# Optimization experiments

Measured on AMD Instinct MI355X. Metric: run time of the kernel, lower is better.

## Reference

```python
import jax, jax.numpy as jnp
import numpy as np

HEADS = 16  # module init arg `heads`


def setup_inputs() -> dict:
    key = jax.random.key(0)
    k1, k2, k3 = jax.random.split(key, 3)
    B, T, D = 2, 2048, 1024
    x = jax.random.normal(k1, (B, T, D), dtype=jnp.float32)
    w_qkv = jax.random.normal(k2, (D, 3 * D), dtype=jnp.float32) * (1.0 / np.sqrt(D))
    w_proj = jax.random.normal(k3, (D, D), dtype=jnp.float32) * (1.0 / np.sqrt(D))
    b_proj = jnp.zeros((D,), dtype=jnp.float32)
    return {"x": x, "w_qkv": w_qkv, "w_proj": w_proj, "b_proj": b_proj,
            "window": 16, "stride": 16}


def reference(x, w_qkv, w_proj, b_proj, window, stride):
    B, T, D = x.shape
    H = HEADS
    hd = D // H
    scale = 1.0 / np.sqrt(hd)

    qkv = x @ w_qkv                              # [B,T,3D]
    qkv = qkv.reshape(B, T, 3, H, hd)
    q = jnp.transpose(qkv[:, :, 0], (0, 2, 1, 3))  # [B,H,T,hd]
    k = jnp.transpose(qkv[:, :, 1], (0, 2, 1, 3))
    v = jnp.transpose(qkv[:, :, 2], (0, 2, 1, 3))

    # Local window attention: pad front with zeros (matches F.pad), gather
    # sliding windows so patches[..., t, w, :] = k_padded[..., t + w, :].
    pad = window - 1
    k_pad = jnp.pad(k, ((0, 0), (0, 0), (pad, 0), (0, 0)))
    v_pad = jnp.pad(v, ((0, 0), (0, 0), (pad, 0), (0, 0)))
    win_idx = jnp.arange(T)[:, None] + jnp.arange(window)[None, :]  # [T,W]
    pk = k_pad[:, :, win_idx]                    # [B,H,T,W,hd]
    pv = v_pad[:, :, win_idx]                    # [B,H,T,W,hd]

    attn_local = jnp.einsum('bhtd,bhtwd->bhtw', q, pk) * scale
    attn_local = jax.nn.softmax(attn_local, axis=-1)  # zero-pad keys included, as in torch
    out_local = jnp.einsum('bhtw,bhtwd->bhtd', attn_local, pv)

    # Strided global attention
    g_idx = jnp.arange(0, T, stride)
    kg = k[:, :, g_idx]                          # [B,H,G,hd]
    vg = v[:, :, g_idx]
    attn_g = jnp.einsum('bhtd,bhgd->bhtg', q, kg) * scale
    attn_g = jax.nn.softmax(attn_g, axis=-1)
    out_global = jnp.einsum('bhtg,bhgd->bhtd', attn_g, vg)

    out = out_local + out_global                 # [B,H,T,hd]
    out = jnp.transpose(out, (0, 2, 1, 3)).reshape(B, T, D)
    return out @ w_proj + b_proj
```

## Files before the change

### kernel.cpp

```cpp
#include <hip/hip_runtime.h>
#include <hip/hip_bf16.h>

#define BB 2
#define TT 2048
#define DD 1024
#define HH 16
#define HD 64
#define WIN 16
#define NG 128
#define QKVLD 3072

typedef __bf16 bf16x8 __attribute__((ext_vector_type(8)));
typedef float f32x4 __attribute__((ext_vector_type(4)));
typedef _Float16 h2 __attribute__((ext_vector_type(2)));

__device__ __forceinline__ unsigned short f2bf(float f) {
    union { float f; unsigned int i; } x; x.f = f;
    unsigned int r = x.i + 0x7FFFu + ((x.i >> 16) & 1u);
    return (unsigned short)(r >> 16);
}
__device__ __forceinline__ unsigned short f2h(float f) {
    union { _Float16 h; unsigned short u; } x; x.h = (_Float16)f; return x.u;
}
__device__ __forceinline__ h2 shfl_h2(h2 v, int mask) {
    union { h2 h; int i; } X; X.h = v;
    X.i = __shfl_xor(X.i, mask, 64);
    return X.h;
}

#if defined(__has_builtin)
#  if __has_builtin(__builtin_amdgcn_fdot2)
#    define DOT2(a, b, c) __builtin_amdgcn_fdot2((a), (b), (c), false)
#  endif
#endif
#ifndef DOT2
#  define DOT2(a, b, c) ((c) + (float)(a).x * (float)(b).x + (float)(a).y * (float)(b).y)
#endif

__device__ __forceinline__ void gll16(const unsigned short* g, unsigned short* l) {
    __builtin_amdgcn_global_load_lds(
        (const __attribute__((address_space(1))) void*)g,
        (__attribute__((address_space(3))) void*)l,
        16, 0, 0);
}

__global__ __launch_bounds__(256) void prepass_kernel(
    const float* __restrict__ x,
    const float* __restrict__ w_qkv,
    const float* __restrict__ w_proj,
    unsigned short* __restrict__ xb,
    unsigned short* __restrict__ wqkvT,
    unsigned short* __restrict__ wprojT)
{
    __shared__ float tile[64][65];
    const int bid = blockIdx.x;
    const int tid = threadIdx.x;

    if (bid < 2048) {
        const size_t i = ((size_t)bid * 256 + tid) * 8;
        float4 f0 = *(const float4*)(x + i);
        float4 f1 = *(const float4*)(x + i + 4);
        ushort4 a = { f2bf(f0.x), f2bf(f0.y), f2bf(f0.z), f2bf(f0.w) };
        ushort4 b = { f2bf(f1.x), f2bf(f1.y), f2bf(f1.z), f2bf(f1.w) };
        *(ushort4*)(xb + i) = a;
        *(ushort4*)(xb + i + 4) = b;
        return;
    }

    const float* w;
    unsigned short* wT;
    int nblk, kblk, N;
    if (bid < 2816) {
        const int b2 = bid - 2048;
        w = w_qkv; wT = wqkvT; N = 3072;
        nblk = b2 % 48; kblk = b2 / 48;
    } else {
        const int b2 = bid - 2816;
        w = w_proj; wT = wprojT; N = 1024;
        nblk = b2 % 16; kblk = b2 / 16;
    }
    const int K = 1024;
    const int n0 = nblk * 64, k0 = kblk * 64;

    {
        const int krow = tid >> 2;
        const int nc0  = (tid & 3) * 16;
        const float* src = w + (size_t)(k0 + krow) * N + n0 + nc0;
        float4 f0 = *(const float4*)(src);
        float4 f1 = *(const float4*)(src + 4);
        float4 f2 = *(const float4*)(src + 8);
        float4 f3 = *(const float4*)(src + 12);
        *(float4*)&tile[krow][nc0]      = f0;
        *(float4*)&tile[krow][nc0 + 4]  = f1;
        *(float4*)&tile[krow][nc0 + 8]  = f2;
        *(float4*)&tile[krow][nc0 + 12] = f3;
    }
    __syncthreads();
    #pragma unroll
    for (int rep = 0; rep < 2; ++rep) {
        const int n   = (tid >> 3) + rep * 32;
        const int kc0 = (tid & 7) * 8;
        union { uint4 v; unsigned short u[8]; } o;
        #pragma unroll
        for (int j = 0; j < 8; ++j) o.u[j] = f2bf(tile[kc0 + j][n]);
        *(uint4*)(wT + (size_t)(n0 + n) * K + k0 + kc0) = o.v;
    }
}

template<int MODE, int TN>
__global__ __launch_bounds__(256) void gemm_kernel(
    const unsigned short* __restrict__ A,
    const unsigned short* __restrict__ Bt,
    void* __restrict__ Cp,
    const float* __restrict__ bias,
    int M, int N, int K)
{
    constexpr int NJ = TN / 32;
    constexpr int BR = TN / 4;
    __shared__ __align__(16) unsigned short As[128 * 32];
    __shared__ __align__(16) unsigned short Bs[TN * 32];
    const int tid  = threadIdx.x;
    const int wave = tid >> 6;
    const int lane = tid & 63;
    const int lm   = lane & 15;
    const int quad = lane >> 4;
    const int wm   = (wave >> 1) * 64;
    const int wn   = (wave & 1) * (TN / 2);
    const int bm   = blockIdx.y * 128;
    const int bn   = blockIdx.x * TN;

    f32x4 acc[4][NJ];
    const f32x4 z4 = { 0.f, 0.f, 0.f, 0.f };
    #pragma unroll
    for (int i = 0; i < 4; ++i)
        #pragma unroll
        for (int j = 0; j < NJ; ++j) acc[i][j] = z4;

    const int lrow = lane >> 2, lcol = (lane & 3) * 8;
    const unsigned short* gA0 = A  + (size_t)(bm + wave * 32 + lrow) * K + lcol;
    const unsigned short* gA1 = gA0 + (size_t)16 * K;
    const unsigned short* gB0 = Bt + (size_t)(bn + wave * BR + lrow) * K + lcol;
    const unsigned short* gB1 = gB0 + (size_t)16 * K;
    unsigned short* lA0 = &As[(wave * 32) * 32];
    unsigned short* lA1 = &As[(wave * 32 + 16) * 32];
    unsigned short* lB0 = &Bs[(wave * BR) * 32];
    unsigned short* lB1 = &Bs[(wave * BR + 16) * 32];

    for (int k0 = 0; k0 < K; k0 += 32) {
        __syncthreads();
        gll16(gA0 + k0, lA0);
        gll16(gA1 + k0, lA1);
        gll16(gB0 + k0, lB0);
        if constexpr (BR == 32) gll16(gB1 + k0, lB1);
        __syncthreads();
        bf16x8 af[4], bfr[NJ];
        #pragma unroll
        for (int i = 0; i < 4; ++i)
            af[i] = *(const bf16x8*)&As[(wm + i * 16 + lm) * 32 + quad * 8];
        #pragma unroll
        for (int j = 0; j < NJ; ++j)
            bfr[j] = *(const bf16x8*)&Bs[(wn + j * 16 + lm) * 32 + quad * 8];
        #pragma unroll
        for (int i = 0; i < 4; ++i)
            #pragma unroll
            for (int j = 0; j < NJ; ++j)
                acc[i][j] = __builtin_amdgcn_mfma_f32_16x16x32_bf16(
                    af[i], bfr[j], acc[i][j], 0, 0, 0);
    }

    #pragma unroll
    for (int i = 0; i < 4; ++i) {
        #pragma unroll
        for (int r = 0; r < 4; ++r) {
            const int row = bm + wm + i * 16 + quad * 4 + r;
            #pragma unroll
            for (int j = 0; j < NJ; ++j) {
                const int col = bn + wn + j * 16 + lm;
                float v = acc[i][j][r];
                if constexpr (MODE == 0) {
                    ((unsigned short*)Cp)[(size_t)row * N + col] = f2h(v);
                } else {
                    ((float*)Cp)[(size_t)row * N + col] = v + bias[col];
                }
            }
        }
    }
}

__global__ __launch_bounds__(256) void attn_kernel(
    const unsigned short* __restrict__ qkv,
    unsigned short* __restrict__ attn_out)
{
    __shared__ __align__(16) unsigned short smem[72 * (2 * 128 + 2 * 47)];
    unsigned short* Kg = smem;
    unsigned short* Vg = smem + 128 * 72;
    unsigned short* Kl = smem + 2 * 128 * 72;
    unsigned short* Vl = Kl + 47 * 72;

    const int tid   = threadIdx.x;
    const int bx    = blockIdx.x;
    const int chunk = bx & 63;
    const int bh    = bx >> 6;
    const int b     = bh >> 4;
    const int h     = bh & 15;
    const int t0    = chunk * 32;
    const int qloc  = tid >> 3;
    const int ks    = tid & 7;
    const int tq    = t0 + qloc;

    const size_t rowK = (size_t)(b * TT) * QKVLD + 1024 + h * HD;

    {
        const int r = tid >> 1, hfi = tid & 1;
        const int g = ((r & 15) << 3) | (r >> 4);
        const unsigned short* kr = qkv + rowK + (size_t)g * 16 * QKVLD + hfi * 32;
        const unsigned short* vr = kr + 1024;
        unsigned short* kd = Kg + r * 72 + hfi * 32;
        unsigned short* vd = Vg + r * 72 + hfi * 32;
        #pragma unroll
        for (int j = 0; j < 4; ++j) {
            *(uint4*)(kd + j * 8) = *(const uint4*)(kr + j * 8);
            *(uint4*)(vd + j * 8) = *(const uint4*)(vr + j * 8);
        }
        if (r < 47) {
            const int t = t0 + r - 15;
            unsigned short* kld = Kl + r * 72 + hfi * 32;
            unsigned short* vld = Vl + r * 72 + hfi * 32;
            if (t < 0) {
                uint4 z = { 0, 0, 0, 0 };
                #pragma unroll
                for (int j = 0; j < 4; ++j) { *(uint4*)(kld + j * 8) = z; *(uint4*)(vld + j * 8) = z; }
            } else {
                const unsigned short* klr = qkv + rowK + (size_t)t * QKVLD + hfi * 32;
                const unsigned short* vlr = klr + 1024;
                #pragma unroll
                for (int j = 0; j < 4; ++j) {
                    *(uint4*)(kld + j * 8) = *(const uint4*)(klr + j * 8);
                    *(uint4*)(vld + j * 8) = *(const uint4*)(vlr + j * 8);
                }
            }
        }
    }

    h2 qh[32];
    {
        const unsigned short* qrow = qkv + (size_t)(b * TT + tq) * QKVLD + h * HD;
        const h2 sc = { (_Float16)0.125f, (_Float16)0.125f };
        #pragma unroll
        for (int i = 0; i < 8; ++i) {
            union { uint4 u; h2 hh[4]; } U;
            U.u = *(const uint4*)(qrow + i * 8);
            qh[4 * i + 0] = U.hh[0] * sc; qh[4 * i + 1] = U.hh[1] * sc;
            qh[4 * i + 2] = U.hh[2] * sc; qh[4 * i + 3] = U.hh[3] * sc;
        }
    }

    __syncthreads();

    auto score = [&](const unsigned short* kp) -> float {
        float s0 = 0.f, s1 = 0.f, s2 = 0.f, s3 = 0.f;
        #pragma unroll
        for (int c = 0; c < 8; ++c) {
            union { uint4 u; h2 hh[4]; } U;
            U.u = *(const uint4*)(kp + c * 8);
            s0 = DOT2(U.hh[0], qh[4 * c + 0], s0);
            s1 = DOT2(U.hh[1], qh[4 * c + 1], s1);
            s2 = DOT2(U.hh[2], qh[4 * c + 2], s2);
            s3 = DOT2(U.hh[3], qh[4 * c + 3], s3);
        }
        return (s0 + s1) + (s2 + s3);
    };

    h2 out2[32];
    #pragma unroll
    for (int i = 0; i < 32; ++i) out2[i] = (h2){ (_Float16)0.f, (_Float16)0.f };

    float pl0 = __expf(score(Kl + (qloc + 2 * ks + 0) * 72));
    float pl1 = __expf(score(Kl + (qloc + 2 * ks + 1) * 72));
    float den = pl0 + pl1;
    den += __shfl_xor(den, 1, 64);
    den += __shfl_xor(den, 2, 64);
    den += __shfl_xor(den, 4, 64);
    const float inv = 1.f / den;
    #pragma unroll
    for (int w = 0; w < 2; ++w) {
        const float pn = (w ? pl1 : pl0) * inv;
        h2 ph; ph.x = (_Float16)pn; ph.y = ph.x;
        const unsigned short* vp = Vl + (qloc + 2 * ks + w) * 72;
        #pragma unroll
        for (int c = 0; c < 8; ++c) {
            union { uint4 u; h2 hh[4]; } U;
            U.u = *(const uint4*)(vp + c * 8);
            out2[4 * c + 0] += ph * U.hh[0]; out2[4 * c + 1] += ph * U.hh[1];
            out2[4 * c + 2] += ph * U.hh[2]; out2[4 * c + 3] += ph * U.hh[3];
        }
    }

    float pg[16];
    float deng = 0.f;
    #pragma unroll
    for (int i = 0; i < 16; ++i) {
        const int g = ks * 16 + i;
        const int row = ((g & 7) << 4) | (g >> 3);
        const float e = __expf(score(Kg + row * 72));
        pg[i] = e; deng += e;
    }
    deng += __shfl_xor(deng, 1, 64);
    deng += __shfl_xor(deng, 2, 64);
    deng += __shfl_xor(deng, 4, 64);
    const float invg = 1.f / deng;
    #pragma unroll
    for (int i = 0; i < 16; ++i) {
        const int g = ks * 16 + i;
        const int row = ((g & 7) << 4) | (g >> 3);
        const float pn = pg[i] * invg;
        h2 ph; ph.x = (_Float16)pn; ph.y = ph.x;
        const unsigned short* vp = Vg + row * 72;
        #pragma unroll
        for (int c = 0; c < 8; ++c) {
            union { uint4 u; h2 hh[4]; } U;
            U.u = *(const uint4*)(vp + c * 8);
            out2[4 * c + 0] += ph * U.hh[0]; out2[4 * c + 1] += ph * U.hh[1];
            out2[4 * c + 2] += ph * U.hh[2]; out2[4 * c + 3] += ph * U.hh[3];
        }
    }

    h2 a[16];
    {
        const bool hi = (ks & 4) != 0;
        #pragma unroll
        for (int i = 0; i < 16; ++i) {
            h2 snd  = hi ? out2[i] : out2[i + 16];
            h2 rcv  = shfl_h2(snd, 4);
            a[i] = (hi ? out2[i + 16] : out2[i]) + rcv;
        }
    }
    h2 bb[8];
    {
        const bool hi = (ks & 2) != 0;
        #pragma unroll
        for (int i = 0; i < 8; ++i) {
            h2 snd  = hi ? a[i] : a[i + 8];
            h2 rcv  = shfl_h2(snd, 2);
            bb[i] = (hi ? a[i + 8] : a[i]) + rcv;
        }
    }
    h2 c4[4];
    {
        const bool hi = (ks & 1) != 0;
        #pragma unroll
        for (int i = 0; i < 4; ++i) {
            h2 snd  = hi ? bb[i] : bb[i + 4];
            h2 rcv  = shfl_h2(snd, 1);
            c4[i] = (hi ? bb[i + 4] : bb[i]) + rcv;
        }
    }

    {
        unsigned int pk[4];
        #pragma unroll
        for (int j = 0; j < 4; ++j)
            pk[j] = (unsigned int)f2bf((float)c4[j].x) | ((unsigned int)f2bf((float)c4[j].y) << 16);
        uint4 st = { pk[0], pk[1], pk[2], pk[3] };
        *(uint4*)(attn_out + (size_t)(b * TT + tq) * DD + h * HD + ks * 8) = st;
    }
}

extern "C" void kernel_launch(void* const* d_in, const int* in_sizes, int n_in,
                              void* d_out, int out_size, void* d_ws, size_t ws_size,
                              hipStream_t stream) {
    const float* x      = (const float*)d_in[0];
    const float* w_qkv  = (const float*)d_in[1];
    const float* w_proj = (const float*)d_in[2];
    const float* b_proj = (const float*)d_in[3];

    char* ws = (char*)d_ws;
    unsigned short* qkv    = (unsigned short*)ws;
    unsigned short* xb     = (unsigned short*)(ws + 25165824);
    unsigned short* attnb  = xb;
    unsigned short* wqkvT  = (unsigned short*)(ws + 25165824 + 8388608);
    unsigned short* wprojT = (unsigned short*)(ws + 25165824 + 8388608 + 6291456);
    float* out = (float*)d_out;

    prepass_kernel<<<3072, 256, 0, stream>>>(x, w_qkv, w_proj, xb, wqkvT, wprojT);

    gemm_kernel<0, 128><<<dim3(3072 / 128, 4096 / 128), 256, 0, stream>>>(
        xb, wqkvT, qkv, nullptr, 4096, 3072, 1024);

    attn_kernel<<<dim3(BB * HH * (TT / 32)), 256, 0, stream>>>(qkv, attnb);

    gemm_kernel<1, 64><<<dim3(1024 / 64, 4096 / 128), 256, 0, stream>>>(
        attnb, wprojT, out, b_proj, 4096, 1024, 1024);
}
```

Baseline: 180.1 us.

## Rewrite attention kernel with MFMA for scores and probability-value products

Replaces the scalar fdot2/packed-fp16 attention inner loops with 16x16x32 f16 MFMA instructions for both QK^T (global and local windows) and P·V. Each block now handles 64 queries with one wave per 16 queries, staging probabilities and transposed V in reused shared memory. Local-window masking is done in the score tile instead of per-thread windows. It aims to cut the VALU-bound attention cost, at the price of extra LDS transposes, more barriers and wasted MFMA work on masked local entries.

Result: faster. 158.6 us (-11.9%).

```diff
diff --git a/kernel.cpp b/kernel.cpp
--- a/kernel.cpp
+++ b/kernel.cpp
@@ -11,6 +11,7 @@
 #define QKVLD 3072
 
 typedef __bf16 bf16x8 __attribute__((ext_vector_type(8)));
+typedef _Float16 f16x8 __attribute__((ext_vector_type(8)));
 typedef float f32x4 __attribute__((ext_vector_type(4)));
 typedef _Float16 h2 __attribute__((ext_vector_type(2)));
 
@@ -22,20 +23,6 @@
 __device__ __forceinline__ unsigned short f2h(float f) {
     union { _Float16 h; unsigned short u; } x; x.h = (_Float16)f; return x.u;
 }
-__device__ __forceinline__ h2 shfl_h2(h2 v, int mask) {
-    union { h2 h; int i; } X; X.h = v;
-    X.i = __shfl_xor(X.i, mask, 64);
-    return X.h;
-}
-
-#if defined(__has_builtin)
-#  if __has_builtin(__builtin_amdgcn_fdot2)
-#    define DOT2(a, b, c) __builtin_amdgcn_fdot2((a), (b), (c), false)
-#  endif
-#endif
-#ifndef DOT2
-#  define DOT2(a, b, c) ((c) + (float)(a).x * (float)(b).x + (float)(a).y * (float)(b).y)
-#endif
 
 __device__ __forceinline__ void gll16(const unsigned short* g, unsigned short* l) {
     __builtin_amdgcn_global_load_lds(
@@ -187,182 +174,191 @@
     }
 }
 
-__global__ __launch_bounds__(256) void attn_kernel(
+__global__ __launch_bounds__(256, 3) void attn_kernel(
     const unsigned short* __restrict__ qkv,
     unsigned short* __restrict__ attn_out)
 {
-    __shared__ __align__(16) unsigned short smem[72 * (2 * 128 + 2 * 47)];
-    unsigned short* Kg = smem;
-    unsigned short* Vg = smem + 128 * 72;
-    unsigned short* Kl = smem + 2 * 128 * 72;
-    unsigned short* Vl = Kl + 47 * 72;
-
-    const int tid   = threadIdx.x;
-    const int bx    = blockIdx.x;
-    const int chunk = bx & 63;
-    const int bh    = bx >> 6;
-    const int b     = bh >> 4;
-    const int h     = bh & 15;
-    const int t0    = chunk * 32;
-    const int qloc  = tid >> 3;
-    const int ks    = tid & 7;
-    const int tq    = t0 + qloc;
-
-    const size_t rowK = (size_t)(b * TT) * QKVLD + 1024 + h * HD;
-
-    {
-        const int r = tid >> 1, hfi = tid & 1;
-        const int g = ((r & 15) << 3) | (r >> 4);
-        const unsigned short* kr = qkv + rowK + (size_t)g * 16 * QKVLD + hfi * 32;
-        const unsigned short* vr = kr + 1024;
-        unsigned short* kd = Kg + r * 72 + hfi * 32;
-        unsigned short* vd = Vg + r * 72 + hfi * 32;
-        #pragma unroll
-        for (int j = 0; j < 4; ++j) {
-            *(uint4*)(kd + j * 8) = *(const uint4*)(kr + j * 8);
-            *(uint4*)(vd + j * 8) = *(const uint4*)(vr + j * 8);
-        }
-        if (r < 47) {
-            const int t = t0 + r - 15;
-            unsigned short* kld = Kl + r * 72 + hfi * 32;
-            unsigned short* vld = Vl + r * 72 + hfi * 32;
-            if (t < 0) {
-                uint4 z = { 0, 0, 0, 0 };
+    __shared__ __align__(16) unsigned short smem[25728];
+    unsigned short* const Kg  = smem;
+    unsigned short* const Kl  = smem + 9216;
+    unsigned short* const VgT = smem;
+    unsigned short* const VlT = smem + 8704;
+    unsigned short* const Pb  = smem + 14976;
+
+    const int tid  = threadIdx.x;
+    const int wave = tid >> 6;
+    const int lane = tid & 63;
+    const int lm   = lane & 15;
+    const int quad = lane >> 4;
+    const int bx   = blockIdx.x;
+    const int bh   = bx >> 5;
+    const int t0   = (bx & 31) * 64;
+    const int b    = bh >> 4;
+    const int h    = bh & 15;
+
+    const size_t baseQ = (size_t)(b * TT) * QKVLD + h * HD;
+
+    const int r  = tid >> 1;
+    const int hf = tid & 1;
+    uint4 vg[4], vl[4];
+    {
+        const unsigned short* ks = qkv + baseQ + 1024 + (size_t)(16 * r) * QKVLD + hf * 32;
+        const unsigned short* vs = ks + 1024;
+        unsigned short* kd = Kg + r * 72 + hf * 32;
+        #pragma unroll
+        for (int j = 0; j < 4; ++j) *(uint4*)(kd + j * 8) = *(const uint4*)(ks + j * 8);
+        #pragma unroll
+        for (int j = 0; j < 4; ++j) vg[j] = *(const uint4*)(vs + j * 8);
+
+        if (r < 80) {
+            const int tl = t0 - 15 + r;
+            unsigned short* kld = Kl + r * 72 + hf * 32;
+            if (tl < 0 || tl >= TT) {
+                const uint4 z = { 0, 0, 0, 0 };
                 #pragma unroll
-                for (int j = 0; j < 4; ++j) { *(uint4*)(kld + j * 8) = z; *(uint4*)(vld + j * 8) = z; }
+                for (int j = 0; j < 4; ++j) { *(uint4*)(kld + j * 8) = z; vl[j] = z; }
             } else {
-                const unsigned short* klr = qkv + rowK + (size_t)t * QKVLD + hfi * 32;
-                const unsigned short* vlr = klr + 1024;
+                const unsigned short* kls = qkv + baseQ + 1024 + (size_t)tl * QKVLD + hf * 32;
+                const unsigned short* vls = kls + 1024;
                 #pragma unroll
-                for (int j = 0; j < 4; ++j) {
-                    *(uint4*)(kld + j * 8) = *(const uint4*)(klr + j * 8);
-                    *(uint4*)(vld + j * 8) = *(const uint4*)(vlr + j * 8);
-                }
+                for (int j = 0; j < 4; ++j) *(uint4*)(kld + j * 8) = *(const uint4*)(kls + j * 8);
+                #pragma unroll
+                for (int j = 0; j < 4; ++j) vl[j] = *(const uint4*)(vls + j * 8);
             }
         }
     }
 
-    h2 qh[32];
-    {
-        const unsigned short* qrow = qkv + (size_t)(b * TT + tq) * QKVLD + h * HD;
+    f16x8 qf[2];
+    {
+        const unsigned short* qrow = qkv + baseQ + (size_t)(t0 + 16 * wave + lm) * QKVLD;
         const h2 sc = { (_Float16)0.125f, (_Float16)0.125f };
         #pragma unroll
-        for (int i = 0; i < 8; ++i) {
-            union { uint4 u; h2 hh[4]; } U;
-            U.u = *(const uint4*)(qrow + i * 8);
-            qh[4 * i + 0] = U.hh[0] * sc; qh[4 * i + 1] = U.hh[1] * sc;
-            qh[4 * i + 2] = U.hh[2] * sc; qh[4 * i + 3] = U.hh[3] * sc;
+        for (int c = 0; c < 2; ++c) {
+            union { uint4 u; h2 hh[4]; f16x8 v; } U;
+            U.u = *(const uint4*)(qrow + c * 32 + quad * 8);
+            #pragma unroll
+            for (int k = 0; k < 4; ++k) U.hh[k] *= sc;
+            qf[c] = U.v;
         }
     }
 
     __syncthreads();
 
-    auto score = [&](const unsigned short* kp) -> float {
-        float s0 = 0.f, s1 = 0.f, s2 = 0.f, s3 = 0.f;
-        #pragma unroll
-        for (int c = 0; c < 8; ++c) {
-            union { uint4 u; h2 hh[4]; } U;
-            U.u = *(const uint4*)(kp + c * 8);
-            s0 = DOT2(U.hh[0], qh[4 * c + 0], s0);
-            s1 = DOT2(U.hh[1], qh[4 * c + 1], s1);
-            s2 = DOT2(U.hh[2], qh[4 * c + 2], s2);
-            s3 = DOT2(U.hh[3], qh[4 * c + 3], s3);
-        }
-        return (s0 + s1) + (s2 + s3);
-    };
-
-    h2 out2[32];
-    #pragma unroll
-    for (int i = 0; i < 32; ++i) out2[i] = (h2){ (_Float16)0.f, (_Float16)0.f };
-
-    float pl0 = __expf(score(Kl + (qloc + 2 * ks + 0) * 72));
-    float pl1 = __expf(score(Kl + (qloc + 2 * ks + 1) * 72));
-    float den = pl0 + pl1;
-    den += __shfl_xor(den, 1, 64);
-    den += __shfl_xor(den, 2, 64);
-    den += __shfl_xor(den, 4, 64);
-    const float inv = 1.f / den;
-    #pragma unroll
-    for (int w = 0; w < 2; ++w) {
-        const float pn = (w ? pl1 : pl0) * inv;
-        h2 ph; ph.x = (_Float16)pn; ph.y = ph.x;
-        const unsigned short* vp = Vl + (qloc + 2 * ks + w) * 72;
-        #pragma unroll
-        for (int c = 0; c < 8; ++c) {
-            union { uint4 u; h2 hh[4]; } U;
-            U.u = *(const uint4*)(vp + c * 8);
-            out2[4 * c + 0] += ph * U.hh[0]; out2[4 * c + 1] += ph * U.hh[1];
-            out2[4 * c + 2] += ph * U.hh[2]; out2[4 * c + 3] += ph * U.hh[3];
-        }
-    }
-
-    float pg[16];
-    float deng = 0.f;
-    #pragma unroll
-    for (int i = 0; i < 16; ++i) {
-        const int g = ks * 16 + i;
-        const int row = ((g & 7) << 4) | (g >> 3);
-        const float e = __expf(score(Kg + row * 72));
-        pg[i] = e; deng += e;
-    }
-    deng += __shfl_xor(deng, 1, 64);
-    deng += __shfl_xor(deng, 2, 64);
-    deng += __shfl_xor(deng, 4, 64);
-    const float invg = 1.f / deng;
-    #pragma unroll
-    for (int i = 0; i < 16; ++i) {
-        const int g = ks * 16 + i;
-        const int row = ((g & 7) << 4) | (g >> 3);
-        const float pn = pg[i] * invg;
-        h2 ph; ph.x = (_Float16)pn; ph.y = ph.x;
-        const unsigned short* vp = Vg + row * 72;
-        #pragma unroll
-        for (int c = 0; c < 8; ++c) {
-            union { uint4 u; h2 hh[4]; } U;
-            U.u = *(const uint4*)(vp + c * 8);
-            out2[4 * c + 0] += ph * U.hh[0]; out2[4 * c + 1] += ph * U.hh[1];
-            out2[4 * c + 2] += ph * U.hh[2]; out2[4 * c + 3] += ph * U.hh[3];
-        }
-    }
-
-    h2 a[16];
-    {
-        const bool hi = (ks & 4) != 0;
-        #pragma unroll
-        for (int i = 0; i < 16; ++i) {
-            h2 snd  = hi ? out2[i] : out2[i + 16];
-            h2 rcv  = shfl_h2(snd, 4);
-            a[i] = (hi ? out2[i + 16] : out2[i]) + rcv;
-        }
-    }
-    h2 bb[8];
-    {
-        const bool hi = (ks & 2) != 0;
-        #pragma unroll
-        for (int i = 0; i < 8; ++i) {
-            h2 snd  = hi ? a[i] : a[i + 8];
-            h2 rcv  = shfl_h2(snd, 2);
-            bb[i] = (hi ? a[i + 8] : a[i]) + rcv;
-        }
-    }
-    h2 c4[4];
-    {
-        const bool hi = (ks & 1) != 0;
-        #pragma unroll
-        for (int i = 0; i < 4; ++i) {
-            h2 snd  = hi ? bb[i] : bb[i + 4];
-            h2 rcv  = shfl_h2(snd, 1);
-            c4[i] = (hi ? bb[i + 4] : bb[i]) + rcv;
-        }
-    }
-
-    {
-        unsigned int pk[4];
-        #pragma unroll
-        for (int j = 0; j < 4; ++j)
-            pk[j] = (unsigned int)f2bf((float)c4[j].x) | ((unsigned int)f2bf((float)c4[j].y) << 16);
-        uint4 st = { pk[0], pk[1], pk[2], pk[3] };
-        *(uint4*)(attn_out + (size_t)(b * TT + tq) * DD + h * HD + ks * 8) = st;
+    f32x4 sg[8], sl[2];
+    const f32x4 z4 = { 0.f, 0.f, 0.f, 0.f };
+    #pragma unroll
+    for (int f = 0; f < 8; ++f) sg[f] = z4;
+    sl[0] = z4; sl[1] = z4;
+    #pragma unroll
+    for (int f = 0; f < 8; ++f)
+        #pragma unroll
+        for (int c = 0; c < 2; ++c)
+            sg[f] = __builtin_amdgcn_mfma_f32_16x16x32_f16(
+                qf[c], *(const f16x8*)&Kg[(16 * f + lm) * 72 + c * 32 + quad * 8],
+                sg[f], 0, 0, 0);
+    #pragma unroll
+    for (int f = 0; f < 2; ++f)
+        #pragma unroll
+        for (int c = 0; c < 2; ++c)
+            sl[f] = __builtin_amdgcn_mfma_f32_16x16x32_f16(
+                qf[c], *(const f16x8*)&Kl[(16 * wave + 16 * f + lm) * 72 + c * 32 + quad * 8],
+                sl[f], 0, 0, 0);
+
+    unsigned short* const Pw = Pb + wave * (16 * 168);
+    float invg[4], invl[4];
+    {
+        float dg[4], dl[4];
+        #pragma unroll
+        for (int rr = 0; rr < 4; ++rr) {
+            float s = 0.f;
+            #pragma unroll
+            for (int f = 0; f < 8; ++f) { float e = __expf(sg[f][rr]); sg[f][rr] = e; s += e; }
+            dg[rr] = s;
+            const int q = quad * 4 + rr;
+            float s2 = 0.f;
+            #pragma unroll
+            for (int f = 0; f < 2; ++f) {
+                const int j2 = 16 * f + lm;
+                float e = (j2 >= q && j2 <= q + 15) ? __expf(sl[f][rr]) : 0.f;
+                sl[f][rr] = e; s2 += e;
+            }
+            dl[rr] = s2;
+        }
+        #pragma unroll
+        for (int m = 1; m <= 8; m <<= 1) {
+            #pragma unroll
+            for (int rr = 0; rr < 4; ++rr) {
+                dg[rr] += __shfl_xor(dg[rr], m, 64);
+                dl[rr] += __shfl_xor(dl[rr], m, 64);
+            }
+        }
+        #pragma unroll
+        for (int rr = 0; rr < 4; ++rr) { invg[rr] = 1.f / dg[rr]; invl[rr] = 1.f / dl[rr]; }
+    }
+
+    #pragma unroll
+    for (int rr = 0; rr < 4; ++rr) {
+        unsigned short* prow = Pw + (quad * 4 + rr) * 168;
+        #pragma unroll
+        for (int f = 0; f < 8; ++f) prow[16 * f + lm] = f2h(sg[f][rr] * invg[rr]);
+        #pragma unroll
+        for (int f = 0; f < 2; ++f) prow[128 + 16 * f + lm] = f2h(sl[f][rr] * invl[rr]);
+    }
+
+    __syncthreads();
+
+    {
+        union { uint4 u[4]; unsigned short s[32]; } Ug;
+        #pragma unroll
+        for (int j = 0; j < 4; ++j) Ug.u[j] = vg[j];
+        #pragma unroll
+        for (int j = 0; j < 32; ++j) VgT[(hf * 32 + j) * 136 + r] = Ug.s[j];
+        if (r < 80) {
+            union { uint4 u[4]; unsigned short s[32]; } Ul;
+            #pragma unroll
+            for (int j = 0; j < 4; ++j) Ul.u[j] = vl[j];
+            #pragma unroll
+            for (int j = 0; j < 32; ++j) VlT[(hf * 32 + j) * 88 + r] = Ul.s[j];
+        }
+    }
+
+    __syncthreads();
+
+    f32x4 o[4];
+    #pragma unroll
+    for (int c = 0; c < 4; ++c) o[c] = z4;
+    #pragma unroll
+    for (int kc = 0; kc < 4; ++kc) {
+        const f16x8 pa = *(const f16x8*)&Pw[lm * 168 + kc * 32 + quad * 8];
+        #pragma unroll
+        for (int c = 0; c < 4; ++c)
+            o[c] = __builtin_amdgcn_mfma_f32_16x16x32_f16(
+                pa, *(const f16x8*)&VgT[(16 * c + lm) * 136 + kc * 32 + quad * 8],
+                o[c], 0, 0, 0);
+    }
+    {
+        const f16x8 pa = *(const f16x8*)&Pw[lm * 168 + 128 + quad * 8];
+        #pragma unroll
+        for (int c = 0; c < 4; ++c)
+            o[c] = __builtin_amdgcn_mfma_f32_16x16x32_f16(
+                pa, *(const f16x8*)&VlT[(16 * c + lm) * 88 + 16 * wave + quad * 8],
+                o[c], 0, 0, 0);
+    }
+
+    #pragma unroll
+    for (int rr = 0; rr < 4; ++rr) {
+        unsigned short* orow_p = Pw + (quad * 4 + rr) * 72;
+        #pragma unroll
+        for (int c = 0; c < 4; ++c) orow_p[16 * c + lm] = f2bf(o[c][rr]);
+    }
+    {
+        const int orow = lane >> 2;
+        const int ocol = (lane & 3) * 16;
+        const uint4 d0 = *(const uint4*)&Pw[orow * 72 + ocol];
+        const uint4 d1 = *(const uint4*)&Pw[orow * 72 + ocol + 8];
+        unsigned short* dst = attn_out + (size_t)(b * TT + t0 + 16 * wave + orow) * DD + h * HD + ocol;
+        *(uint4*)(dst)     = d0;
+        *(uint4*)(dst + 8) = d1;
     }
 }
 
@@ -387,7 +383,7 @@
     gemm_kernel<0, 128><<<dim3(3072 / 128, 4096 / 128), 256, 0, stream>>>(
         xb, wqkvT, qkv, nullptr, 4096, 3072, 1024);
 
-    attn_kernel<<<dim3(BB * HH * (TT / 32)), 256, 0, stream>>>(qkv, attnb);
+    attn_kernel<<<dim3(BB * HH * (TT / 64)), 256, 0, stream>>>(qkv, attnb);
 
     gemm_kernel<1, 64><<<dim3(1024 / 64, 4096 / 128), 256, 0, stream>>>(
         attnb, wprojT, out, b_proj, 4096, 1024, 1024);
```
